# Kernel tuning notes

Measured on AMD Instinct MI355X. Metric: run time of the kernel, lower is better.

The kernel has to match this reference:

```python
import jax, jax.numpy as jnp
import numpy as np

N_NODES = 100000
N_EDGES = 1600000
D_IN = 128
D_OUT = 128


def setup_inputs() -> dict:
    key = jax.random.key(0)
    k_x, k_r, k_c, k_v, k_w = jax.random.split(key, 5)
    X = jax.random.normal(k_x, (N_NODES, D_IN), dtype=jnp.float32)
    A_rows = jax.random.randint(k_r, (N_EDGES,), 0, N_NODES, dtype=jnp.int32)
    A_cols = jax.random.randint(k_c, (N_EDGES,), 0, N_NODES, dtype=jnp.int32)
    A_vals = jax.random.uniform(k_v, (N_EDGES,), dtype=jnp.float32)
    # Xavier-uniform linear weight [out, in], zero bias (matches reset_parameters)
    limit = float(np.sqrt(6.0 / (D_IN + D_OUT)))
    W = jax.random.uniform(k_w, (D_OUT, D_IN), dtype=jnp.float32, minval=-limit, maxval=limit)
    b = jnp.zeros((D_OUT,), dtype=jnp.float32)
    return {"X": X, "A_rows": A_rows, "A_cols": A_cols, "A_vals": A_vals, "W": W, "b": b}


def reference(X, A_rows, A_cols, A_vals, W, b):
    # h = A_sparse @ X  (COO SpMM: gather neighbor features, scale, scatter-add by row)
    msgs = A_vals[:, None] * X[A_cols]          # [E, D_IN]
    h = jax.ops.segment_sum(msgs, A_rows, num_segments=N_NODES)  # [N, D_IN]
    # dense linear projection
    return h @ W.T + b
```

## Files before the change

### kernel.cpp

```cpp
#include <hip/hip_runtime.h>

#define N_NODES_C 100000
#define N_EDGES_C 1600000
#define D_C 128
#define NBKT 1563
#define RPB 64
#define CAP 1536
#define PTILE 4096
#define NPB ((N_EDGES_C + PTILE - 1) / PTILE)
#define NGB ((N_NODES_C + 63) / 64)
#define WB_STRIDE 136

static __device__ __forceinline__ unsigned short f2bf(float x) {
    unsigned u = __float_as_uint(x);
    unsigned r = 0x7fffu + ((u >> 16) & 1u);
    return (unsigned short)((u + r) >> 16);
}
static __device__ __forceinline__ float bflo(unsigned u) { return __uint_as_float(u << 16); }
static __device__ __forceinline__ float bfhi(unsigned u) { return __uint_as_float(u & 0xffff0000u); }

typedef __attribute__((ext_vector_type(8))) __bf16 bf16x8;
typedef __attribute__((ext_vector_type(4))) float f32x4;
union FragU { uint4 u; bf16x8 b; };

__global__ __launch_bounds__(256) void prep(const float* __restrict__ W,
                                            const float* __restrict__ b,
                                            unsigned short* __restrict__ Wbf,
                                            int* __restrict__ gcount,
                                            float* __restrict__ pbias) {
    int t = blockIdx.x * 256 + threadIdx.x;
    if (t < 4096) {
        float4 w = ((const float4*)W)[t];
        uint2 p;
        p.x = (unsigned)f2bf(w.x) | ((unsigned)f2bf(w.y) << 16);
        p.y = (unsigned)f2bf(w.z) | ((unsigned)f2bf(w.w) << 16);
        ((uint2*)Wbf)[t] = p;
    } else if (t < 4096 + NBKT) {
        gcount[t - 4096] = 0;
    } else {
        int k = t - (4096 + NBKT);
        if (k < 128) pbias[k] = b[(k & 7) * 16 + (k >> 3)];
    }
}

union SMemF {
    struct {
        int lhist[NBKT];
        int lbase[NBKT];
        unsigned short ebkt[PTILE];
        unsigned short ernk[PTILE];
    } part;
    unsigned short wb[128 * WB_STRIDE];
};

__global__ __launch_bounds__(256) void fused(const float* __restrict__ X,
                                             const int* __restrict__ rows,
                                             const int* __restrict__ cols,
                                             const float* __restrict__ vals,
                                             const unsigned short* __restrict__ Wbf,
                                             int* __restrict__ gcount,
                                             int2* __restrict__ staging,
                                             unsigned short* __restrict__ Y,
                                             int n, int E) {
    __shared__ SMemF sm;
    const int tid = threadIdx.x;

    if (blockIdx.x < NPB) {
        const int t0 = blockIdx.x * PTILE;

        for (int i = tid; i < NBKT; i += 256) sm.part.lhist[i] = 0;
        __syncthreads();

#pragma unroll
        for (int k = 0; k < PTILE / 256; ++k) {
            int e = t0 + k * 256 + tid;
            if (e < E) {
                int bkt = rows[e] >> 6;
                int rnk = atomicAdd(&sm.part.lhist[bkt], 1);
                sm.part.ebkt[k * 256 + tid] = (unsigned short)bkt;
                sm.part.ernk[k * 256 + tid] = (unsigned short)rnk;
            }
        }
        __syncthreads();

        for (int i = tid; i < NBKT; i += 256)
            sm.part.lbase[i] = sm.part.lhist[i] ? atomicAdd(&gcount[i], sm.part.lhist[i]) : 0;
        __syncthreads();

#pragma unroll
        for (int k = 0; k < PTILE / 256; ++k) {
            int e = t0 + k * 256 + tid;
            if (e < E) {
                int li = k * 256 + tid;
                int bkt = sm.part.ebkt[li];
                int dst = sm.part.lbase[bkt] + sm.part.ernk[li];
                if (dst < CAP) {
                    int rl = rows[e] & (RPB - 1);
                    int2 p;
                    p.x = cols[e] | (rl << 17);
                    p.y = __float_as_int(vals[e]);
                    staging[(long)bkt * CAP + dst] = p;
                }
            }
        }
        return;
    }

    const int g = blockIdx.x - NPB;
    const int wave = tid >> 6;
    const int lane = tid & 63;
    const int m16 = lane & 15;
    const int quad = lane >> 4;

    for (int i = tid; i < 128 * 16; i += 256) {
        int o = i >> 4;
        int k8 = (i & 15) * 8;
        *(uint4*)&sm.wb[o * WB_STRIDE + k8] = *(const uint4*)&Wbf[o * D_C + k8];
    }

    const int row0 = g * 64 + wave * 16;
    int row = row0 + m16;
    int rowc = (row < n) ? row : (n - 1);

    FragU a[4];
    const float* xp = X + (long)rowc * D_C + quad * 8;
#pragma unroll
    for (int s = 0; s < 4; ++s) {
        float4 x0 = *(const float4*)(xp + s * 32);
        float4 x1 = *(const float4*)(xp + s * 32 + 4);
        a[s].u.x = (unsigned)f2bf(x0.x) | ((unsigned)f2bf(x0.y) << 16);
        a[s].u.y = (unsigned)f2bf(x0.z) | ((unsigned)f2bf(x0.w) << 16);
        a[s].u.z = (unsigned)f2bf(x1.x) | ((unsigned)f2bf(x1.y) << 16);
        a[s].u.w = (unsigned)f2bf(x1.z) | ((unsigned)f2bf(x1.w) << 16);
    }
    __syncthreads();

    f32x4 acc[8];
#pragma unroll
    for (int t = 0; t < 8; ++t) acc[t] = (f32x4){0.f, 0.f, 0.f, 0.f};

#pragma unroll
    for (int s = 0; s < 4; ++s) {
#pragma unroll
        for (int t = 0; t < 8; ++t) {
            FragU bf;
            bf.u = *(const uint4*)&sm.wb[(t * 16 + m16) * WB_STRIDE + s * 32 + quad * 8];
            acc[t] = __builtin_amdgcn_mfma_f32_16x16x32_bf16(a[s].b, bf.b, acc[t], 0, 0, 0);
        }
    }

#pragma unroll
    for (int r = 0; r < 4; ++r) {
        int orow = row0 + quad * 4 + r;
        if (orow < n) {
            uint4 v;
            v.x = (unsigned)f2bf(acc[0][r]) | ((unsigned)f2bf(acc[1][r]) << 16);
            v.y = (unsigned)f2bf(acc[2][r]) | ((unsigned)f2bf(acc[3][r]) << 16);
            v.z = (unsigned)f2bf(acc[4][r]) | ((unsigned)f2bf(acc[5][r]) << 16);
            v.w = (unsigned)f2bf(acc[6][r]) | ((unsigned)f2bf(acc[7][r]) << 16);
            *(uint4*)&Y[(long)orow * D_C + m16 * 8] = v;
        }
    }
}

__global__ __launch_bounds__(256) void sort_aggregate(const int* __restrict__ gcount,
                                                      const int2* __restrict__ staging,
                                                      const unsigned short* __restrict__ Y,
                                                      const float* __restrict__ pbias,
                                                      float* __restrict__ out, int n) {
    __shared__ int2 pl[CAP];
    __shared__ int hist[RPB];
    __shared__ int lcur[RPB];
    __shared__ int rbegL[RPB];
    __shared__ int rcntL[RPB];

    const int bb = blockIdx.x, tid = threadIdx.x;
    int cnt = gcount[bb];
    if (cnt > CAP) cnt = CAP;
    const long s = (long)bb * CAP;

    if (tid < RPB) hist[tid] = 0;
    __syncthreads();

    int2 p_reg[6];
#pragma unroll
    for (int k = 0; k < 6; ++k) {
        int i = k * 256 + tid;
        if (i < cnt) p_reg[k] = staging[s + i];
    }
#pragma unroll
    for (int k = 0; k < 6; ++k) {
        int i = k * 256 + tid;
        if (i < cnt) atomicAdd(&hist[((unsigned)p_reg[k].x) >> 17], 1);
    }
    __syncthreads();

    int v = (tid < RPB) ? hist[tid] : 0;
    for (int off = 1; off < RPB; off <<= 1) {
        int t = (tid >= off && tid < RPB) ? hist[tid - off] : 0;
        __syncthreads();
        if (tid < RPB) hist[tid] += t;
        __syncthreads();
    }
    if (tid < RPB) {
        int excl = hist[tid] - v;
        lcur[tid] = excl;
        rbegL[tid] = excl;
        rcntL[tid] = v;
    }
    __syncthreads();

#pragma unroll
    for (int k = 0; k < 6; ++k) {
        int i = k * 256 + tid;
        if (i < cnt) {
            int rl = ((unsigned)p_reg[k].x) >> 17;
            int slot = atomicAdd(&lcur[rl], 1);
            pl[slot] = p_reg[k];
        }
    }
    __syncthreads();

    const int lane = tid & 15;
    const unsigned short* Yl = Y + lane * 8;
    float4 b0 = *(const float4*)&pbias[lane * 8];
    float4 b1 = *(const float4*)&pbias[lane * 8 + 4];

#pragma unroll
    for (int pass = 0; pass < RPB / 16; ++pass) {
        int rlocal = pass * 16 + (tid >> 4);
        int row = bb * RPB + rlocal;
        if (row >= n) continue;

        int i = rbegL[rlocal];
        int e = i + rcntL[rlocal];

        float acc[8];
        acc[0] = b0.x; acc[1] = b0.y; acc[2] = b0.z; acc[3] = b0.w;
        acc[4] = b1.x; acc[5] = b1.y; acc[6] = b1.z; acc[7] = b1.w;

        for (; i + 8 <= e; i += 8) {
            int2 p[8];
            uint4 y[8];
#pragma unroll
            for (int u = 0; u < 8; ++u) p[u] = pl[i + u];
#pragma unroll
            for (int u = 0; u < 8; ++u)
                y[u] = *(const uint4*)&Yl[(long)(p[u].x & 0x1FFFF) * D_C];
#pragma unroll
            for (int u = 0; u < 8; ++u) {
                float v2 = __int_as_float(p[u].y);
                acc[0] += v2 * bflo(y[u].x); acc[1] += v2 * bfhi(y[u].x);
                acc[2] += v2 * bflo(y[u].y); acc[3] += v2 * bfhi(y[u].y);
                acc[4] += v2 * bflo(y[u].z); acc[5] += v2 * bfhi(y[u].z);
                acc[6] += v2 * bflo(y[u].w); acc[7] += v2 * bfhi(y[u].w);
            }
        }
        for (; i + 4 <= e; i += 4) {
            int2 p[4];
            uint4 y[4];
#pragma unroll
            for (int u = 0; u < 4; ++u) p[u] = pl[i + u];
#pragma unroll
            for (int u = 0; u < 4; ++u)
                y[u] = *(const uint4*)&Yl[(long)(p[u].x & 0x1FFFF) * D_C];
#pragma unroll
            for (int u = 0; u < 4; ++u) {
                float v2 = __int_as_float(p[u].y);
                acc[0] += v2 * bflo(y[u].x); acc[1] += v2 * bfhi(y[u].x);
                acc[2] += v2 * bflo(y[u].y); acc[3] += v2 * bfhi(y[u].y);
                acc[4] += v2 * bflo(y[u].z); acc[5] += v2 * bfhi(y[u].z);
                acc[6] += v2 * bflo(y[u].w); acc[7] += v2 * bfhi(y[u].w);
            }
        }
        for (; i < e; ++i) {
            int2 p = pl[i];
            uint4 y = *(const uint4*)&Yl[(long)(p.x & 0x1FFFF) * D_C];
            float v2 = __int_as_float(p.y);
            acc[0] += v2 * bflo(y.x); acc[1] += v2 * bfhi(y.x);
            acc[2] += v2 * bflo(y.y); acc[3] += v2 * bfhi(y.y);
            acc[4] += v2 * bflo(y.z); acc[5] += v2 * bfhi(y.z);
            acc[6] += v2 * bflo(y.w); acc[7] += v2 * bfhi(y.w);
        }

        float* op = out + (long)row * D_C + lane;
#pragma unroll
        for (int j = 0; j < 8; ++j)
            __builtin_nontemporal_store(acc[j], op + j * 16);
    }
}

__global__ __launch_bounds__(256) void gemm_mfma(const float* __restrict__ X,
                                                 const float* __restrict__ W,
                                                 unsigned short* __restrict__ Y, int n) {
    __shared__ unsigned short Wb[128 * WB_STRIDE];

    const int tid = threadIdx.x;
    const int wave = tid >> 6;
    const int lane = tid & 63;
    const int m16 = lane & 15;
    const int quad = lane >> 4;

    const int row0 = blockIdx.x * 64 + wave * 16;
    int row = row0 + m16;
    int rowc = (row < n) ? row : (n - 1);

    float4 xv[4][2];
    const float* xp = X + (long)rowc * D_C + quad * 8;
#pragma unroll
    for (int s = 0; s < 4; ++s) {
        xv[s][0] = *(const float4*)(xp + s * 32);
        xv[s][1] = *(const float4*)(xp + s * 32 + 4);
    }

    for (int i = tid; i < 128 * 32; i += 256) {
        int o = i >> 5;
        int k4 = (i & 31) * 4;
        float4 w = *(const float4*)&W[o * 128 + k4];
        uint2 p;
        p.x = (unsigned)f2bf(w.x) | ((unsigned)f2bf(w.y) << 16);
        p.y = (unsigned)f2bf(w.z) | ((unsigned)f2bf(w.w) << 16);
        *(uint2*)&Wb[o * WB_STRIDE + k4] = p;
    }
    __syncthreads();

    FragU a[4];
#pragma unroll
    for (int s = 0; s < 4; ++s) {
        a[s].u.x = (unsigned)f2bf(xv[s][0].x) | ((unsigned)f2bf(xv[s][0].y) << 16);
        a[s].u.y = (unsigned)f2bf(xv[s][0].z) | ((unsigned)f2bf(xv[s][0].w) << 16);
        a[s].u.z = (unsigned)f2bf(xv[s][1].x) | ((unsigned)f2bf(xv[s][1].y) << 16);
        a[s].u.w = (unsigned)f2bf(xv[s][1].z) | ((unsigned)f2bf(xv[s][1].w) << 16);
    }

    f32x4 acc[8];
#pragma unroll
    for (int t = 0; t < 8; ++t) acc[t] = (f32x4){0.f, 0.f, 0.f, 0.f};

#pragma unroll
    for (int s = 0; s < 4; ++s) {
#pragma unroll
        for (int t = 0; t < 8; ++t) {
            FragU bf;
            bf.u = *(const uint4*)&Wb[(t * 16 + m16) * WB_STRIDE + s * 32 + quad * 8];
            acc[t] = __builtin_amdgcn_mfma_f32_16x16x32_bf16(a[s].b, bf.b, acc[t], 0, 0, 0);
        }
    }

#pragma unroll
    for (int t = 0; t < 8; ++t) {
#pragma unroll
        for (int r = 0; r < 4; ++r) {
            int orow = row0 + quad * 4 + r;
            if (orow < n) Y[(long)orow * D_C + t * 16 + m16] = f2bf(acc[t][r]);
        }
    }
}

__global__ __launch_bounds__(256) void init_out(const float* __restrict__ b,
                                                float* __restrict__ out, int n) {
    int idx = blockIdx.x * 256 + threadIdx.x;
    int total = n * (D_C / 4);
    if (idx < total) {
        int o4 = idx & (D_C / 4 - 1);
        ((float4*)out)[idx] = ((const float4*)b)[o4];
    }
}

__global__ __launch_bounds__(256) void scatter_edges(const int* __restrict__ rows,
                                                     const int* __restrict__ cols,
                                                     const float* __restrict__ vals,
                                                     const unsigned short* __restrict__ Y,
                                                     float* __restrict__ out, int E) {
    int e = blockIdx.x * 8 + (threadIdx.x >> 5);
    if (e >= E) return;
    int lane = threadIdx.x & 31;
    int row = rows[e];
    int col = cols[e];
    float v = vals[e];
    uint2 y = *(const uint2*)&Y[(long)col * D_C + lane * 4];
    float* dst = out + (long)row * D_C + lane * 4;
    unsafeAtomicAdd(dst + 0, v * bflo(y.x));
    unsafeAtomicAdd(dst + 1, v * bfhi(y.x));
    unsafeAtomicAdd(dst + 2, v * bflo(y.y));
    unsafeAtomicAdd(dst + 3, v * bfhi(y.y));
}

extern "C" void kernel_launch(void* const* d_in, const int* in_sizes, int n_in,
                              void* d_out, int out_size, void* d_ws, size_t ws_size,
                              hipStream_t stream) {
    const float* X  = (const float*)d_in[0];
    const int*   Ar = (const int*)d_in[1];
    const int*   Ac = (const int*)d_in[2];
    const float* Av = (const float*)d_in[3];
    const float* W  = (const float*)d_in[4];
    const float* b  = (const float*)d_in[5];
    float* out = (float*)d_out;

    unsigned short* Y = (unsigned short*)d_ws;
    int2* staging = (int2*)(Y + 12800000);
    unsigned short* Wbf = (unsigned short*)(staging + (size_t)NBKT * CAP);
    int* gcount = (int*)(Wbf + 16384);
    float* pbias = (float*)(gcount + NBKT);
    size_t need = (size_t)12800000 * 2 + (size_t)NBKT * CAP * 8 + 32768 +
                  (size_t)NBKT * 4 + 512;

    if (ws_size >= need) {
        prep<<<23, 256, 0, stream>>>(W, b, Wbf, gcount, pbias);
        fused<<<NPB + NGB, 256, 0, stream>>>(X, Ar, Ac, Av, Wbf, gcount, staging, Y,
                                             N_NODES_C, N_EDGES_C);
        sort_aggregate<<<NBKT, 256, 0, stream>>>(gcount, staging, Y, pbias, out, N_NODES_C);
    } else {
        gemm_mfma<<<(N_NODES_C + 63) / 64, 256, 0, stream>>>(X, W, Y, N_NODES_C);
        init_out<<<(N_NODES_C * (D_C / 4) + 255) / 256, 256, 0, stream>>>(b, out, N_NODES_C);
        scatter_edges<<<(N_EDGES_C + 7) / 8, 256, 0, stream>>>(Ar, Ac, Av, Y, out, N_EDGES_C);
    }
}
```

Baseline: 219.4 us.

## Pre-swizzle W into MFMA fragment order and process 128 rows per GEMM block

The prep kernel now writes bf16 W already laid out in MFMA B-fragment order, so the GEMM blocks copy it linearly into shared memory and each lane reads contiguous 16-byte fragments with no padded stride. Each GEMM block now covers 128 rows in two 64-row passes, halving the number of GEMM blocks and the per-block W staging cost. The trade-off is less GEMM parallelism and a serial second pass whose X loads are not overlapped with the first pass's MFMAs.

```diff
diff --git a/kernel.cpp b/kernel.cpp
--- a/kernel.cpp
+++ b/kernel.cpp
@@ -8,7 +8,8 @@
 #define CAP 1536
 #define PTILE 4096
 #define NPB ((N_EDGES_C + PTILE - 1) / PTILE)
-#define NGB ((N_NODES_C + 63) / 64)
+#define GROWS 128
+#define NGB ((N_NODES_C + GROWS - 1) / GROWS)
 #define WB_STRIDE 136
 
 static __device__ __forceinline__ unsigned short f2bf(float x) {
@@ -29,16 +30,23 @@
                                             int* __restrict__ gcount,
                                             float* __restrict__ pbias) {
     int t = blockIdx.x * 256 + threadIdx.x;
-    if (t < 4096) {
-        float4 w = ((const float4*)W)[t];
-        uint2 p;
-        p.x = (unsigned)f2bf(w.x) | ((unsigned)f2bf(w.y) << 16);
-        p.y = (unsigned)f2bf(w.z) | ((unsigned)f2bf(w.w) << 16);
-        ((uint2*)Wbf)[t] = p;
-    } else if (t < 4096 + NBKT) {
-        gcount[t - 4096] = 0;
+    if (t < 2048) {
+        int lane = t & 63;
+        int fs = (t >> 6) & 3;
+        int tt = t >> 8;
+        const float* src = W + (tt * 16 + (lane & 15)) * D_C + fs * 32 + (lane >> 4) * 8;
+        float4 w0 = *(const float4*)(src);
+        float4 w1 = *(const float4*)(src + 4);
+        uint4 v;
+        v.x = (unsigned)f2bf(w0.x) | ((unsigned)f2bf(w0.y) << 16);
+        v.y = (unsigned)f2bf(w0.z) | ((unsigned)f2bf(w0.w) << 16);
+        v.z = (unsigned)f2bf(w1.x) | ((unsigned)f2bf(w1.y) << 16);
+        v.w = (unsigned)f2bf(w1.z) | ((unsigned)f2bf(w1.w) << 16);
+        *(uint4*)&Wbf[t * 8] = v;
+    } else if (t < 2048 + NBKT) {
+        gcount[t - 2048] = 0;
     } else {
-        int k = t - (4096 + NBKT);
+        int k = t - (2048 + NBKT);
         if (k < 128) pbias[k] = b[(k & 7) * 16 + (k >> 3)];
     }
 }
@@ -50,7 +58,7 @@
         unsigned short ebkt[PTILE];
         unsigned short ernk[PTILE];
     } part;
-    unsigned short wb[128 * WB_STRIDE];
+    unsigned short wb[16384];
 };
 
 __global__ __launch_bounds__(256) void fused(const float* __restrict__ X,
@@ -112,53 +120,71 @@
     const int m16 = lane & 15;
     const int quad = lane >> 4;
 
-    for (int i = tid; i < 128 * 16; i += 256) {
-        int o = i >> 4;
-        int k8 = (i & 15) * 8;
-        *(uint4*)&sm.wb[o * WB_STRIDE + k8] = *(const uint4*)&Wbf[o * D_C + k8];
-    }
-
-    const int row0 = g * 64 + wave * 16;
-    int row = row0 + m16;
-    int rowc = (row < n) ? row : (n - 1);
+    for (int i = tid; i < 2048; i += 256)
+        *(uint4*)&sm.wb[i * 8] = *(const uint4*)&Wbf[i * 8];
+
+    const int grow0 = g * GROWS;
 
     FragU a[4];
-    const float* xp = X + (long)rowc * D_C + quad * 8;
-#pragma unroll
-    for (int s = 0; s < 4; ++s) {
-        float4 x0 = *(const float4*)(xp + s * 32);
-        float4 x1 = *(const float4*)(xp + s * 32 + 4);
-        a[s].u.x = (unsigned)f2bf(x0.x) | ((unsigned)f2bf(x0.y) << 16);
-        a[s].u.y = (unsigned)f2bf(x0.z) | ((unsigned)f2bf(x0.w) << 16);
-        a[s].u.z = (unsigned)f2bf(x1.x) | ((unsigned)f2bf(x1.y) << 16);
-        a[s].u.w = (unsigned)f2bf(x1.z) | ((unsigned)f2bf(x1.w) << 16);
-    }
-    __syncthreads();
-
-    f32x4 acc[8];
-#pragma unroll
-    for (int t = 0; t < 8; ++t) acc[t] = (f32x4){0.f, 0.f, 0.f, 0.f};
-
-#pragma unroll
-    for (int s = 0; s < 4; ++s) {
-#pragma unroll
-        for (int t = 0; t < 8; ++t) {
-            FragU bf;
-            bf.u = *(const uint4*)&sm.wb[(t * 16 + m16) * WB_STRIDE + s * 32 + quad * 8];
-            acc[t] = __builtin_amdgcn_mfma_f32_16x16x32_bf16(a[s].b, bf.b, acc[t], 0, 0, 0);
-        }
-    }
-
-#pragma unroll
-    for (int r = 0; r < 4; ++r) {
-        int orow = row0 + quad * 4 + r;
-        if (orow < n) {
-            uint4 v;
-            v.x = (unsigned)f2bf(acc[0][r]) | ((unsigned)f2bf(acc[1][r]) << 16);
-            v.y = (unsigned)f2bf(acc[2][r]) | ((unsigned)f2bf(acc[3][r]) << 16);
-            v.z = (unsigned)f2bf(acc[4][r]) | ((unsigned)f2bf(acc[5][r]) << 16);
-            v.w = (unsigned)f2bf(acc[6][r]) | ((unsigned)f2bf(acc[7][r]) << 16);
-            *(uint4*)&Y[(long)orow * D_C + m16 * 8] = v;
+    {
+        int row = grow0 + wave * 16 + m16;
+        int rowc = (row < n) ? row : (n - 1);
+        const float* xp = X + (long)rowc * D_C + quad * 8;
+#pragma unroll
+        for (int s = 0; s < 4; ++s) {
+            float4 x0 = *(const float4*)(xp + s * 32);
+            float4 x1 = *(const float4*)(xp + s * 32 + 4);
+            a[s].u.x = (unsigned)f2bf(x0.x) | ((unsigned)f2bf(x0.y) << 16);
+            a[s].u.y = (unsigned)f2bf(x0.z) | ((unsigned)f2bf(x0.w) << 16);
+            a[s].u.z = (unsigned)f2bf(x1.x) | ((unsigned)f2bf(x1.y) << 16);
+            a[s].u.w = (unsigned)f2bf(x1.z) | ((unsigned)f2bf(x1.w) << 16);
+        }
+    }
+    __syncthreads();
+
+#pragma unroll
+    for (int rt = 0; rt < 2; ++rt) {
+        const int row0 = grow0 + rt * 64 + wave * 16;
+        if (rt) {
+            int row = row0 + m16;
+            int rowc = (row < n) ? row : (n - 1);
+            const float* xp = X + (long)rowc * D_C + quad * 8;
+#pragma unroll
+            for (int s = 0; s < 4; ++s) {
+                float4 x0 = *(const float4*)(xp + s * 32);
+                float4 x1 = *(const float4*)(xp + s * 32 + 4);
+                a[s].u.x = (unsigned)f2bf(x0.x) | ((unsigned)f2bf(x0.y) << 16);
+                a[s].u.y = (unsigned)f2bf(x0.z) | ((unsigned)f2bf(x0.w) << 16);
+                a[s].u.z = (unsigned)f2bf(x1.x) | ((unsigned)f2bf(x1.y) << 16);
+                a[s].u.w = (unsigned)f2bf(x1.z) | ((unsigned)f2bf(x1.w) << 16);
+            }
+        }
+
+        f32x4 acc[8];
+#pragma unroll
+        for (int t = 0; t < 8; ++t) acc[t] = (f32x4){0.f, 0.f, 0.f, 0.f};
+
+#pragma unroll
+        for (int s = 0; s < 4; ++s) {
+#pragma unroll
+            for (int t = 0; t < 8; ++t) {
+                FragU bf;
+                bf.u = *(const uint4*)&sm.wb[(((t * 4 + s) * 64) + lane) * 8];
+                acc[t] = __builtin_amdgcn_mfma_f32_16x16x32_bf16(a[s].b, bf.b, acc[t], 0, 0, 0);
+            }
+        }
+
+#pragma unroll
+        for (int r = 0; r < 4; ++r) {
+            int orow = row0 + quad * 4 + r;
+            if (orow < n) {
+                uint4 v;
+                v.x = (unsigned)f2bf(acc[0][r]) | ((unsigned)f2bf(acc[1][r]) << 16);
+                v.y = (unsigned)f2bf(acc[2][r]) | ((unsigned)f2bf(acc[3][r]) << 16);
+                v.z = (unsigned)f2bf(acc[4][r]) | ((unsigned)f2bf(acc[5][r]) << 16);
+                v.w = (unsigned)f2bf(acc[6][r]) | ((unsigned)f2bf(acc[7][r]) << 16);
+                *(uint4*)&Y[(long)orow * D_C + m16 * 8] = v;
+            }
         }
     }
 }
@@ -406,7 +432,7 @@
                   (size_t)NBKT * 4 + 512;
 
     if (ws_size >= need) {
-        prep<<<23, 256, 0, stream>>>(W, b, Wbf, gcount, pbias);
+        prep<<<15, 256, 0, stream>>>(W, b, Wbf, gcount, pbias);
         fused<<<NPB + NGB, 256, 0, stream>>>(X, Ar, Ac, Av, Wbf, gcount, staging, Y,
                                              N_NODES_C, N_EDGES_C);
         sort_aggregate<<<NBKT, 256, 0, stream>>>(gcount, staging, Y, pbias, out, N_NODES_C);
```

After: 221.5 us. About the same (+1.0%).
